# Optimization experiments

Measured on AMD Instinct MI355X. Metric: run time of the kernel, lower is better.

Reference implementation:

```python
import jax, jax.numpy as jnp
import numpy as np

N_NODES = 100000
N_EDGES = 625000
D_IN = 128
D_OUT = 128
N_ETYPES = 64


def setup_inputs() -> dict:
    key = jax.random.key(0)
    k1, k2, k3, k4, k5, k6 = jax.random.split(key, 6)
    node_features = jax.random.normal(k1, (N_NODES, D_IN), dtype=jnp.float32)
    edge_index = jax.random.randint(k2, (2, N_EDGES), 0, N_NODES, dtype=jnp.int64)
    edge_type = jax.random.randint(k3, (N_EDGES,), 0, N_ETYPES, dtype=jnp.int64)
    edge_emb = jax.random.normal(k4, (N_ETYPES, D_OUT), dtype=jnp.float32)
    W = jax.random.normal(k5, (D_IN, D_OUT), dtype=jnp.float32) / np.sqrt(D_IN)
    b = jax.random.normal(k6, (D_OUT,), dtype=jnp.float32) * 0.01
    return {"node_features": node_features, "edge_index": edge_index,
            "edge_type": edge_type, "edge_emb": edge_emb, "W": W, "b": b}


def reference(node_features, edge_index, edge_type, edge_emb, W, b):
    # Linear transform of node features: (N, D_out)
    h = node_features @ W + b
    src, tgt = edge_index[0], edge_index[1]
    # Per-edge message: gather src feature + edge-type embedding  (E, D_out)
    messages = h[src] + edge_emb[edge_type]
    # Scatter-add into target nodes
    aggregated = jax.ops.segment_sum(messages, tgt, num_segments=N_NODES)
    # Self contribution + ReLU
    return jax.nn.relu(aggregated + h)
```

## Files before the change

### kernel.cpp

```cpp
#include <hip/hip_runtime.h>
#include <hip/hip_bf16.h>

#define D 128

typedef __attribute__((ext_vector_type(8))) short short8v;
typedef __attribute__((ext_vector_type(4))) float float4v;

__device__ __forceinline__ unsigned short f2bf(float f) {
  union { float f; unsigned int u; } v; v.f = f;
  unsigned int r = v.u + 0x7fffu + ((v.u >> 16) & 1u);
  return (unsigned short)(r >> 16);
}
__device__ __forceinline__ unsigned int pkbf(float lo, float hi) {
  float2 f; f.x = lo; f.y = hi;
  __hip_bfloat162 v = __float22bfloat162_rn(f);
  union { __hip_bfloat162 b; unsigned int u; } c; c.b = v;
  return c.u;
}
__device__ __forceinline__ float bflo(unsigned int u) {
  union { unsigned int v; float f; } c; c.v = u << 16; return c.f;
}
__device__ __forceinline__ float bfhi(unsigned int u) {
  union { unsigned int v; float f; } c; c.v = u & 0xffff0000u; return c.f;
}

__global__ __launch_bounds__(256) void prep_kernel(
    const float* __restrict__ W, const float* __restrict__ eemb,
    unsigned short* __restrict__ Wt, unsigned short* __restrict__ em_bf,
    unsigned short* __restrict__ h_bf, int* __restrict__ counts,
    int n_nodes) {
  int i = blockIdx.x * 256 + threadIdx.x;
  if (i < D * D) Wt[i] = f2bf(W[(i & 127) * D + (i >> 7)]);
  if (i < 64 * D) em_bf[i] = f2bf(eemb[i]);
  if (i < 64) ((unsigned int*)(h_bf + (size_t)n_nodes * D))[i] = 0u;
  if (i >= 64 && i < 128) ((unsigned int*)(em_bf + 64 * D))[i - 64] = 0u;
  if (i < n_nodes) counts[i] = 0;
}

__global__ __launch_bounds__(256, 4) void gemm_h_kernel(
    const float* __restrict__ nf, const unsigned short* __restrict__ Wt,
    const float* __restrict__ b, unsigned short* __restrict__ h_bf,
    const int* __restrict__ eidx_tgt, int* __restrict__ counts,
    int n_nodes, int n_edges, int epb) {
  const int tid = threadIdx.x;
  const int wv = tid >> 6;
  const int ln = tid & 63;
  const int m = ln & 15;
  const int q = ln >> 4;
  const int node = blockIdx.x * 64 + wv * 16 + m;
  const int row = node < n_nodes ? node : n_nodes - 1;
  const float4* xr4 = (const float4*)(nf + (size_t)row * D);

  float4 xv[8];
  #pragma unroll
  for (int kc = 0; kc < 4; ++kc) {
    xv[kc * 2]     = xr4[kc * 8 + q * 2];
    xv[kc * 2 + 1] = xr4[kc * 8 + q * 2 + 1];
  }
  short8v bfrag[4];
  #pragma unroll
  for (int kc = 0; kc < 4; ++kc) {
    union { unsigned int u[4]; short8v s; } cv;
    cv.u[0] = pkbf(xv[kc * 2].x, xv[kc * 2].y);
    cv.u[1] = pkbf(xv[kc * 2].z, xv[kc * 2].w);
    cv.u[2] = pkbf(xv[kc * 2 + 1].x, xv[kc * 2 + 1].y);
    cv.u[3] = pkbf(xv[kc * 2 + 1].z, xv[kc * 2 + 1].w);
    bfrag[kc] = cv.s;
  }

  const unsigned short* wbase = Wt + m * D + q * 8;
  short8v aC[4], aN[4];
  #pragma unroll
  for (int kc = 0; kc < 4; ++kc) aC[kc] = *(const short8v*)(wbase + kc * 32);

  float4v acc[8] = {};
  #pragma unroll
  for (int nt = 0; nt < 8; ++nt) {
    if (nt < 7) {
      const unsigned short* wn = wbase + (nt + 1) * 16 * D;
      #pragma unroll
      for (int kc = 0; kc < 4; ++kc) aN[kc] = *(const short8v*)(wn + kc * 32);
    }
    #pragma unroll
    for (int kc = 0; kc < 4; ++kc)
      acc[nt] = __builtin_amdgcn_mfma_f32_16x16x32_bf16(aC[kc], bfrag[kc],
                                                        acc[nt], 0, 0, 0);
    #pragma unroll
    for (int kc = 0; kc < 4; ++kc) aC[kc] = aN[kc];
  }

  if (node < n_nodes) {
    unsigned short* orow = h_bf + (size_t)node * D + q * 4;
    #pragma unroll
    for (int nt = 0; nt < 8; ++nt) {
      const float4 bv = *(const float4*)&b[nt * 16 + q * 4];
      uint2 val;
      val.x = pkbf(acc[nt][0] + bv.x, acc[nt][1] + bv.y);
      val.y = pkbf(acc[nt][2] + bv.z, acc[nt][3] + bv.w);
      *(uint2*)(orow + nt * 16) = val;
    }
  }

  const int ebase = blockIdx.x * epb;
  int eend = ebase + epb;
  if (eend > n_edges) eend = n_edges;
  for (int e = ebase + tid; e < eend; e += 256)
    atomicAdd(&counts[eidx_tgt[e]], 1);
}

__global__ __launch_bounds__(256) void scan1_kernel(
    const int* __restrict__ counts, int* __restrict__ offsets,
    int* __restrict__ blockSums, int n) {
  __shared__ int lds[256];
  const int tid = threadIdx.x;
  const int base = blockIdx.x * 1024 + tid * 4;
  int v[4];
  #pragma unroll
  for (int k = 0; k < 4; ++k) v[k] = (base + k < n) ? counts[base + k] : 0;
  int s = v[0] + v[1] + v[2] + v[3];
  lds[tid] = s;
  for (int off = 1; off < 256; off <<= 1) {
    __syncthreads();
    int t = (tid >= off) ? lds[tid - off] : 0;
    __syncthreads();
    lds[tid] += t;
  }
  __syncthreads();
  int run = lds[tid] - s;
  #pragma unroll
  for (int k = 0; k < 4; ++k) {
    if (base + k < n) offsets[base + k] = run;
    run += v[k];
  }
  if (tid == 255) blockSums[blockIdx.x] = lds[255];
}

__global__ __launch_bounds__(256) void scan23_kernel(
    int* __restrict__ offsets, int* __restrict__ cursor,
    const int* __restrict__ blockSums, int nb, int n, int n_edges) {
  __shared__ int lds[256];
  const int tid = threadIdx.x;
  const int bid = blockIdx.x;
  lds[tid] = (tid < bid && tid < nb) ? blockSums[tid] : 0;
  __syncthreads();
  #pragma unroll
  for (int off = 128; off > 0; off >>= 1) {
    if (tid < off) lds[tid] += lds[tid + off];
    __syncthreads();
  }
  const int add = lds[0];
  const int base = bid * 1024 + tid * 4;
  #pragma unroll
  for (int k = 0; k < 4; ++k) {
    int i = base + k;
    if (i < n) {
      int o = offsets[i] + add;
      offsets[i] = o;
      cursor[i] = o;
    }
  }
  if (bid == 0 && tid == 0) offsets[n] = n_edges;
}

__global__ __launch_bounds__(256) void scatter_kernel(
    const int* __restrict__ eidx, const int* __restrict__ etype,
    int* __restrict__ cursor, unsigned int* __restrict__ packed, int n_edges) {
  const int e0 = (blockIdx.x * 256 + threadIdx.x) * 4;
  if (e0 + 3 < n_edges) {
    const int4 s4 = *(const int4*)&eidx[e0];
    const int4 t4 = *(const int4*)&eidx[n_edges + e0];
    const int4 y4 = *(const int4*)&etype[e0];
    int pos;
    pos = atomicAdd(&cursor[t4.x], 1);
    packed[pos] = (unsigned int)s4.x | ((unsigned int)y4.x << 17);
    pos = atomicAdd(&cursor[t4.y], 1);
    packed[pos] = (unsigned int)s4.y | ((unsigned int)y4.y << 17);
    pos = atomicAdd(&cursor[t4.z], 1);
    packed[pos] = (unsigned int)s4.z | ((unsigned int)y4.z << 17);
    pos = atomicAdd(&cursor[t4.w], 1);
    packed[pos] = (unsigned int)s4.w | ((unsigned int)y4.w << 17);
  } else {
    for (int e = e0; e < n_edges; ++e) {
      const int pos = atomicAdd(&cursor[eidx[n_edges + e]], 1);
      packed[pos] = (unsigned int)eidx[e] | ((unsigned int)etype[e] << 17);
    }
  }
}

__global__ __launch_bounds__(256) void aggregate_kernel(
    const int* __restrict__ offsets, const unsigned int* __restrict__ packed,
    const uint2* __restrict__ e4, const uint2* __restrict__ h4,
    float* __restrict__ out, int n_nodes, int n_edges, unsigned int zero_p) {
  const int gid = blockIdx.x * 256 + threadIdx.x;
  const int lane = threadIdx.x & 63;
  const int half = lane >> 5;
  const int sl = lane & 31;
  const int n = (gid >> 6) * 2 + half;
  if (n >= n_nodes) return;

  const uint2 sb = h4[(size_t)n * 32 + sl];
  float a0 = bflo(sb.x), a1 = bfhi(sb.x), a2 = bflo(sb.y), a3 = bfhi(sb.y);
  float c0 = 0.f, c1 = 0.f, c2 = 0.f, c3 = 0.f;

  int j = offsets[n];
  const int end = offsets[n + 1];
  int trips = (end - j + 3) >> 2;
  int to = __shfl_xor(trips, 32);
  const int T = trips > to ? trips : to;
  const int emax = n_edges - 1;

  for (int t = 0; t < T; ++t, j += 4) {
    const int j1 = j + 1, j2 = j + 2, j3 = j + 3;
    unsigned int p0 = packed[j  <= emax ? j  : emax];
    unsigned int p1 = packed[j1 <= emax ? j1 : emax];
    unsigned int p2 = packed[j2 <= emax ? j2 : emax];
    unsigned int p3 = packed[j3 <= emax ? j3 : emax];
    p0 = (j  < end) ? p0 : zero_p;
    p1 = (j1 < end) ? p1 : zero_p;
    p2 = (j2 < end) ? p2 : zero_p;
    p3 = (j3 < end) ? p3 : zero_p;
    const uint2 g0 = h4[(size_t)(p0 & 0x1FFFFu) * 32 + sl];
    const uint2 g1 = h4[(size_t)(p1 & 0x1FFFFu) * 32 + sl];
    const uint2 g2 = h4[(size_t)(p2 & 0x1FFFFu) * 32 + sl];
    const uint2 g3 = h4[(size_t)(p3 & 0x1FFFFu) * 32 + sl];
    const uint2 e0 = e4[(p0 >> 17) * 32 + sl];
    const uint2 e1 = e4[(p1 >> 17) * 32 + sl];
    const uint2 e2 = e4[(p2 >> 17) * 32 + sl];
    const uint2 e3 = e4[(p3 >> 17) * 32 + sl];
    a0 += bflo(g0.x) + bflo(e0.x); a1 += bfhi(g0.x) + bfhi(e0.x);
    a2 += bflo(g0.y) + bflo(e0.y); a3 += bfhi(g0.y) + bfhi(e0.y);
    c0 += bflo(g1.x) + bflo(e1.x); c1 += bfhi(g1.x) + bfhi(e1.x);
    c2 += bflo(g1.y) + bflo(e1.y); c3 += bfhi(g1.y) + bfhi(e1.y);
    a0 += bflo(g2.x) + bflo(e2.x); a1 += bfhi(g2.x) + bfhi(e2.x);
    a2 += bflo(g2.y) + bflo(e2.y); a3 += bfhi(g2.y) + bfhi(e2.y);
    c0 += bflo(g3.x) + bflo(e3.x); c1 += bfhi(g3.x) + bfhi(e3.x);
    c2 += bflo(g3.y) + bflo(e3.y); c3 += bfhi(g3.y) + bfhi(e3.y);
  }

  float4 r;
  r.x = fmaxf(a0 + c0, 0.f);
  r.y = fmaxf(a1 + c1, 0.f);
  r.z = fmaxf(a2 + c2, 0.f);
  r.w = fmaxf(a3 + c3, 0.f);
  ((float4*)out)[(size_t)n * 32 + sl] = r;
}

extern "C" void kernel_launch(void* const* d_in, const int* in_sizes, int n_in,
                              void* d_out, int out_size, void* d_ws,
                              size_t ws_size, hipStream_t stream) {
  const float* nf   = (const float*)d_in[0];
  const int*   eidx = (const int*)d_in[1];
  const int*   etyp = (const int*)d_in[2];
  const float* eemb = (const float*)d_in[3];
  const float* W    = (const float*)d_in[4];
  const float* b    = (const float*)d_in[5];

  const int n_nodes = in_sizes[0] / D;
  const int n_edges = in_sizes[2];

  float* out = (float*)d_out;

  char* base = (char*)d_ws;
  unsigned short* Wt = (unsigned short*)base;
  unsigned short* em_bf = (unsigned short*)(base + 32768);
  unsigned short* h_bf = (unsigned short*)(base + 65536);
  char* tail = base + 65536 + (size_t)(n_nodes + 1) * D * 2;
  int* counts = (int*)tail;
  int* offsets = counts + n_nodes;
  int* cursor = offsets + (n_nodes + 1);
  int* blockSums = cursor + n_nodes;
  unsigned int* packed = (unsigned int*)(blockSums + 1024);

  const int nb = (n_nodes + 1023) / 1024;
  const int gemmBlocks = (n_nodes + 63) / 64;
  const int epb = (n_edges + gemmBlocks - 1) / gemmBlocks;

  prep_kernel<<<(n_nodes + 255) / 256, 256, 0, stream>>>(W, eemb, Wt, em_bf,
                                                         h_bf, counts, n_nodes);

  gemm_h_kernel<<<gemmBlocks, 256, 0, stream>>>(
      nf, Wt, b, h_bf, eidx + n_edges, counts, n_nodes, n_edges, epb);

  scan1_kernel<<<nb, 256, 0, stream>>>(counts, offsets, blockSums, n_nodes);
  scan23_kernel<<<nb, 256, 0, stream>>>(offsets, cursor, blockSums, nb,
                                        n_nodes, n_edges);

  scatter_kernel<<<(n_edges + 1023) / 1024, 256, 0, stream>>>(
      eidx, etyp, cursor, packed, n_edges);

  const unsigned int zero_p = (unsigned int)n_nodes | (64u << 17);
  const int aggBlocks = (n_nodes + 7) / 8;
  aggregate_kernel<<<aggBlocks, 256, 0, stream>>>(
      offsets, packed, (const uint2*)em_bf, (const uint2*)h_bf, out, n_nodes,
      n_edges, zero_p);
}
```

Before: 138.1 us.

## Make GEMM persistent with resident W halves, prefetched tiles, and dedicated histogram blocks

Turns the node-feature GEMM into a persistent kernel of 768 blocks. Each wave keeps one 64-column half of W in registers and loops over 16-row tiles, double-buffering the next tile's feature loads while it computes the current one. The per-block edge histogram slice is replaced by 192 separate blocks that do only the atomic target counting. This avoids reloading W for every tile and overlaps global loads with MFMA work. It uses more registers (launch bound lowered to 2) and relies on n_nodes being a multiple of 16, since the row clamp was removed.

```diff
diff --git a/kernel.cpp b/kernel.cpp
--- a/kernel.cpp
+++ b/kernel.cpp
@@ -2,6 +2,8 @@
 #include <hip/hip_bf16.h>
 
 #define D 128
+#define GEMM_BLOCKS 768
+#define HIST_BLOCKS 192
 
 typedef __attribute__((ext_vector_type(8))) short short8v;
 typedef __attribute__((ext_vector_type(4))) float float4v;
@@ -37,75 +39,97 @@
   if (i < n_nodes) counts[i] = 0;
 }
 
-__global__ __launch_bounds__(256, 4) void gemm_h_kernel(
+__device__ __forceinline__ void loadx(const float* __restrict__ nf, int t,
+                                      int m, int q, float4 (&xr)[8]) {
+  const float4* xr4 = (const float4*)(nf + (size_t)(t * 16 + m) * D);
+  #pragma unroll
+  for (int kc = 0; kc < 4; ++kc) {
+    xr[kc * 2]     = xr4[kc * 8 + q * 2];
+    xr[kc * 2 + 1] = xr4[kc * 8 + q * 2 + 1];
+  }
+}
+
+__device__ __forceinline__ void compute_store(
+    const float4 (&xr)[8], const short8v (&A)[4][4],
+    const float* __restrict__ b, unsigned short* __restrict__ h_bf,
+    int t, int m, int q, int ch) {
+  short8v bf[4];
+  #pragma unroll
+  for (int kc = 0; kc < 4; ++kc) {
+    union { unsigned int u[4]; short8v s; } cv;
+    cv.u[0] = pkbf(xr[kc * 2].x, xr[kc * 2].y);
+    cv.u[1] = pkbf(xr[kc * 2].z, xr[kc * 2].w);
+    cv.u[2] = pkbf(xr[kc * 2 + 1].x, xr[kc * 2 + 1].y);
+    cv.u[3] = pkbf(xr[kc * 2 + 1].z, xr[kc * 2 + 1].w);
+    bf[kc] = cv.s;
+  }
+  float4v acc[4] = {};
+  #pragma unroll
+  for (int kc = 0; kc < 4; ++kc) {
+    #pragma unroll
+    for (int nt = 0; nt < 4; ++nt)
+      acc[nt] = __builtin_amdgcn_mfma_f32_16x16x32_bf16(A[nt][kc], bf[kc],
+                                                        acc[nt], 0, 0, 0);
+  }
+  unsigned short* orow = h_bf + (size_t)(t * 16 + m) * D + ch * 64 + q * 4;
+  #pragma unroll
+  for (int nt = 0; nt < 4; ++nt) {
+    const float4 bv = *(const float4*)(b + ch * 64 + nt * 16 + q * 4);
+    uint2 val;
+    val.x = pkbf(acc[nt][0] + bv.x, acc[nt][1] + bv.y);
+    val.y = pkbf(acc[nt][2] + bv.z, acc[nt][3] + bv.w);
+    *(uint2*)(orow + nt * 16) = val;
+  }
+}
+
+__global__ __launch_bounds__(256, 2) void gemm_h_kernel(
     const float* __restrict__ nf, const unsigned short* __restrict__ Wt,
     const float* __restrict__ b, unsigned short* __restrict__ h_bf,
     const int* __restrict__ eidx_tgt, int* __restrict__ counts,
-    int n_nodes, int n_edges, int epb) {
+    int n_edges, int n_tiles) {
   const int tid = threadIdx.x;
-  const int wv = tid >> 6;
-  const int ln = tid & 63;
-  const int m = ln & 15;
-  const int q = ln >> 4;
-  const int node = blockIdx.x * 64 + wv * 16 + m;
-  const int row = node < n_nodes ? node : n_nodes - 1;
-  const float4* xr4 = (const float4*)(nf + (size_t)row * D);
-
-  float4 xv[8];
-  #pragma unroll
-  for (int kc = 0; kc < 4; ++kc) {
-    xv[kc * 2]     = xr4[kc * 8 + q * 2];
-    xv[kc * 2 + 1] = xr4[kc * 8 + q * 2 + 1];
-  }
-  short8v bfrag[4];
-  #pragma unroll
-  for (int kc = 0; kc < 4; ++kc) {
-    union { unsigned int u[4]; short8v s; } cv;
-    cv.u[0] = pkbf(xv[kc * 2].x, xv[kc * 2].y);
-    cv.u[1] = pkbf(xv[kc * 2].z, xv[kc * 2].w);
-    cv.u[2] = pkbf(xv[kc * 2 + 1].x, xv[kc * 2 + 1].y);
-    cv.u[3] = pkbf(xv[kc * 2 + 1].z, xv[kc * 2 + 1].w);
-    bfrag[kc] = cv.s;
-  }
-
-  const unsigned short* wbase = Wt + m * D + q * 8;
-  short8v aC[4], aN[4];
-  #pragma unroll
-  for (int kc = 0; kc < 4; ++kc) aC[kc] = *(const short8v*)(wbase + kc * 32);
-
-  float4v acc[8] = {};
-  #pragma unroll
-  for (int nt = 0; nt < 8; ++nt) {
-    if (nt < 7) {
-      const unsigned short* wn = wbase + (nt + 1) * 16 * D;
-      #pragma unroll
-      for (int kc = 0; kc < 4; ++kc) aN[kc] = *(const short8v*)(wn + kc * 32);
-    }
+
+  if (blockIdx.x >= GEMM_BLOCKS) {
+    const int nthr = HIST_BLOCKS * 256;
+    for (int e = (blockIdx.x - GEMM_BLOCKS) * 256 + tid; e < n_edges;
+         e += nthr)
+      atomicAdd(&counts[eidx_tgt[e]], 1);
+    return;
+  }
+
+  const int wv = tid >> 6, ln = tid & 63;
+  const int m = ln & 15, q = ln >> 4;
+  const int wgl = blockIdx.x * 4 + wv;
+  const int pair = wgl >> 1;
+  const int ch = wgl & 1;
+  const int nPairs = GEMM_BLOCKS * 2;
+
+  short8v A[4][4];
+  #pragma unroll
+  for (int nt = 0; nt < 4; ++nt) {
+    const unsigned short* wrow = Wt + (ch * 64 + nt * 16 + m) * D + q * 8;
     #pragma unroll
     for (int kc = 0; kc < 4; ++kc)
-      acc[nt] = __builtin_amdgcn_mfma_f32_16x16x32_bf16(aC[kc], bfrag[kc],
-                                                        acc[nt], 0, 0, 0);
-    #pragma unroll
-    for (int kc = 0; kc < 4; ++kc) aC[kc] = aN[kc];
-  }
-
-  if (node < n_nodes) {
-    unsigned short* orow = h_bf + (size_t)node * D + q * 4;
-    #pragma unroll
-    for (int nt = 0; nt < 8; ++nt) {
-      const float4 bv = *(const float4*)&b[nt * 16 + q * 4];
-      uint2 val;
-      val.x = pkbf(acc[nt][0] + bv.x, acc[nt][1] + bv.y);
-      val.y = pkbf(acc[nt][2] + bv.z, acc[nt][3] + bv.w);
-      *(uint2*)(orow + nt * 16) = val;
-    }
-  }
-
-  const int ebase = blockIdx.x * epb;
-  int eend = ebase + epb;
-  if (eend > n_edges) eend = n_edges;
-  for (int e = ebase + tid; e < eend; e += 256)
-    atomicAdd(&counts[eidx_tgt[e]], 1);
+      A[nt][kc] = *(const short8v*)(wrow + kc * 32);
+  }
+
+  float4 xa[8], xb[8];
+
+  int t = pair;
+  if (t >= n_tiles) return;
+  loadx(nf, t, m, q, xa);
+  while (true) {
+    const int t2 = t + nPairs;
+    if (t2 < n_tiles) loadx(nf, t2, m, q, xb);
+    compute_store(xa, A, b, h_bf, t, m, q, ch);
+    if (t2 >= n_tiles) break;
+    t = t2;
+    const int t3 = t + nPairs;
+    if (t3 < n_tiles) loadx(nf, t3, m, q, xa);
+    compute_store(xb, A, b, h_bf, t, m, q, ch);
+    if (t3 >= n_tiles) break;
+    t = t3;
+  }
 }
 
 __global__ __launch_bounds__(256) void scan1_kernel(
@@ -272,14 +296,13 @@
   unsigned int* packed = (unsigned int*)(blockSums + 1024);
 
   const int nb = (n_nodes + 1023) / 1024;
-  const int gemmBlocks = (n_nodes + 63) / 64;
-  const int epb = (n_edges + gemmBlocks - 1) / gemmBlocks;
+  const int n_tiles = (n_nodes + 15) / 16;
 
   prep_kernel<<<(n_nodes + 255) / 256, 256, 0, stream>>>(W, eemb, Wt, em_bf,
                                                          h_bf, counts, n_nodes);
 
-  gemm_h_kernel<<<gemmBlocks, 256, 0, stream>>>(
-      nf, Wt, b, h_bf, eidx + n_edges, counts, n_nodes, n_edges, epb);
+  gemm_h_kernel<<<GEMM_BLOCKS + HIST_BLOCKS, 256, 0, stream>>>(
+      nf, Wt, b, h_bf, eidx + n_edges, counts, n_edges, n_tiles);
 
   scan1_kernel<<<nb, 256, 0, stream>>>(counts, offsets, blockSums, n_nodes);
   scan23_kernel<<<nb, 256, 0, stream>>>(offsets, cursor, blockSums, nb,
```

After: 131.7 us. 4.6% less time.
